# Kernel tuning notes

Hardware: AMD Instinct MI355X
Metric: run time of the kernel (lower is better)

Reference implementation:

```python
import jax, jax.numpy as jnp
import numpy as np

N_NODES = 100000
N_EDGES = 1600000
N_GRAPHS = 256
D = 128      # d_graph
H = 256      # hidden
VOCAB = 30000
OUT = 2


def setup_inputs() -> dict:
    key = jax.random.key(0)
    ks = jax.random.split(key, 24)
    def lin(k, fin, fout):
        s = 1.0 / np.sqrt(fin)
        kw, kb = jax.random.split(k)
        return (jax.random.uniform(kw, (fin, fout), jnp.float32, -s, s),
                jax.random.uniform(kb, (fout,), jnp.float32, -s, s))
    inp = {
        'feat': jax.random.randint(ks[0], (N_NODES,), 0, VOCAB),
        'src': jax.random.randint(ks[1], (N_EDGES,), 0, N_NODES),
        'dst': jax.random.randint(ks[2], (N_EDGES,), 0, N_NODES),
        'graph_id': jnp.sort(jax.random.randint(ks[3], (N_NODES,), 0, N_GRAPHS)),
        'emb': jax.random.normal(ks[4], (VOCAB, D), jnp.float32),
    }
    # SAGEConv layer 0/1: fc_self + fc_neigh + bias (mean aggregator)
    inp['ws0'], _ = lin(ks[5], D, D)
    inp['wn0'], inp['b0'] = lin(ks[6], D, D)
    inp['ws1'], _ = lin(ks[7], D, D)
    inp['wn1'], inp['b1'] = lin(ks[8], D, D)
    inp['e1_w'], inp['e1_b'] = lin(ks[9], D, H)
    inp['e2_w'], inp['e2_b'] = lin(ks[10], H, H)
    inp['e3_w'], inp['e3_b'] = lin(ks[11], H, H)
    inp['e4_w'], inp['e4_b'] = lin(ks[12], H, H)
    inp['pred_w'], inp['pred_b'] = lin(ks[13], H, OUT)
    return inp


def _sage_mean(h, src, dst, ws, wn, b):
    # gather src features, mean-scatter to dst (DGL SAGEConv 'mean')
    msg = jnp.take(h, src, axis=0)                       # [E, D]
    agg = jax.ops.segment_sum(msg, dst, num_segments=N_NODES)
    deg = jax.ops.segment_sum(jnp.ones((src.shape[0],), h.dtype), dst,
                              num_segments=N_NODES)
    h_neigh = agg / jnp.maximum(deg, 1.0)[:, None]
    return h @ ws + h_neigh @ wn + b


def reference(feat, src, dst, graph_id, emb,
              ws0, wn0, b0, ws1, wn1, b1,
              e1_w, e1_b, e2_w, e2_b, e3_w, e3_b, e4_w, e4_b,
              pred_w, pred_b):
    h = jnp.take(emb, feat, axis=0)                      # [N, D]
    h = jax.nn.relu(_sage_mean(h, src, dst, ws0, wn0, b0))
    h = jax.nn.relu(_sage_mean(h, src, dst, ws1, wn1, b1))
    # dgl.mean_nodes: per-graph mean pool
    gsum = jax.ops.segment_sum(h, graph_id, num_segments=N_GRAPHS)
    gcnt = jax.ops.segment_sum(jnp.ones((N_NODES,), h.dtype), graph_id,
                               num_segments=N_GRAPHS)
    hg = gsum / jnp.maximum(gcnt, 1.0)[:, None]          # [B, D]
    hidden = jax.nn.relu(hg @ e1_w + e1_b)
    h2 = jax.nn.relu(hidden @ e2_w + e2_b)
    h3 = jax.nn.relu(h2 @ e3_w + e3_b)
    h4 = jax.nn.relu(h3 @ e4_w + e4_b)
    y = h4 @ pred_w + pred_b
    return jax.nn.log_softmax(y, axis=1), hidden
```

## Files before the change

### kernel.cpp

```cpp
#include <hip/hip_runtime.h>
#include <hip/hip_bf16.h>
#include <math.h>

#define DF 128
#define HID 256
#define NG 256
#define CSR_CAP 1024

typedef __attribute__((ext_vector_type(8))) short s8v;
typedef __attribute__((ext_vector_type(4))) float f32x4;
typedef __attribute__((ext_vector_type(2))) float f32x2;

__device__ __forceinline__ unsigned pack2bf(float lo, float hi){
  unsigned a = __bfloat16_as_ushort(__float2bfloat16(lo));
  unsigned b = __bfloat16_as_ushort(__float2bfloat16(hi));
  return a | (b<<16);
}

__global__ __launch_bounds__(256)
void k_pre0(const float* __restrict__ emb, unsigned* __restrict__ emb_f8, int nvoc,
            const int* __restrict__ dst, int* __restrict__ gb,
            const int* __restrict__ gid, float* __restrict__ gcnt,
            const float* __restrict__ ws0, const float* __restrict__ wn0,
            const float* __restrict__ ws1, const float* __restrict__ wn1,
            unsigned short* __restrict__ wt,
            int N, int E, int NC){
  __shared__ int hist[256];
  const int b = blockIdx.x, t = threadIdx.x;
  if (b < NC){
    int idx = b*256 + t;
    int total = nvoc*(DF/8);
    if (idx<total){
      const float4* e4 = (const float4*)emb;
      float4 v0 = e4[(size_t)idx*2], v1 = e4[(size_t)idx*2+1];
      unsigned w0 = __builtin_amdgcn_cvt_pk_fp8_f32(v0.x, v0.y, 0, false);
      w0 = __builtin_amdgcn_cvt_pk_fp8_f32(v0.z, v0.w, w0, true);
      unsigned w1 = __builtin_amdgcn_cvt_pk_fp8_f32(v1.x, v1.y, 0, false);
      w1 = __builtin_amdgcn_cvt_pk_fp8_f32(v1.z, v1.w, w1, true);
      ((uint2*)emb_f8)[idx] = make_uint2(w0,w1);
    }
  } else if (b < NC+256){
    int bb = b - NC;
    hist[t]=0; __syncthreads();
    for (int i = bb*256+t; i < E; i += 256*256)
      atomicAdd(&hist[dst[i]>>9], 1);
    __syncthreads();
    if (hist[t]) atomicAdd(&gb[t], hist[t]);
  } else if (b < NC+512){
    int bb = b - (NC+256);
    hist[t]=0; __syncthreads();
    for (int i = bb*256+t; i < N; i += 256*256)
      atomicAdd(&hist[gid[i]], 1);
    __syncthreads();
    if (hist[t]) atomicAdd(&gcnt[t], (float)hist[t]);
  } else {
    int bb = b - (NC+512);
    int n = bb & 127;
    int layer = bb >> 7;
    const float* ws = layer? ws1 : ws0;
    const float* wn = layer? wn1 : wn0;
    float v = (t<128)? ws[t*DF+n] : wn[(t-128)*DF+n];
    wt[((size_t)layer*DF + n)*256 + t] = __bfloat16_as_ushort(__float2bfloat16(v));
  }
}

__global__ __launch_bounds__(256)
void k_mid(const int* __restrict__ feat, const unsigned* __restrict__ emb_f8,
           unsigned* __restrict__ h_f8, int N,
           const int* __restrict__ src, const int* __restrict__ dst,
           const int* __restrict__ gb, int* __restrict__ bcur,
           unsigned* __restrict__ pairs, int E, int NP1){
  const int b = blockIdx.x, t = threadIdx.x;
  if (b < NP1){
    int idx = b*256 + t;
    int total = N*8;
    if (idx<total){
      int i = idx>>3, c = idx&7;
      ((uint4*)h_f8)[idx] = ((const uint4*)emb_f8)[(size_t)feat[i]*8 + c];
    }
    return;
  }
  __shared__ int sgb[256];
  __shared__ int hist[256];
  __shared__ int base[256];
  __shared__ int cur[256];
  const int bb = b - NP1;
  const int CH = (E + 255)/256;
  const int s = bb*CH;
  int e = s+CH; if (e>E) e=E;
  if (s>=E) return;
  int v = gb[t];
  sgb[t]=v;
  hist[t]=0;
  __syncthreads();
  for (int o=1;o<256;o<<=1){
    int x = (t>=o)? sgb[t-o] : 0;
    __syncthreads();
    sgb[t]+=x;
    __syncthreads();
  }
  int bstart = sgb[t]-v;
  for (int i=s+t; i<e; i+=256) atomicAdd(&hist[dst[i]>>9],1);
  __syncthreads();
  if (hist[t]){ base[t] = bstart + atomicAdd(&bcur[t],hist[t]); }
  cur[t]=0;
  __syncthreads();
  for (int i=s+t; i<e; i+=256){
    int d = dst[i];
    int bk = d>>9;
    int r = atomicAdd(&cur[bk],1);
    pairs[base[bk]+r] = ((unsigned)src[i]<<9) | (unsigned)(d & 511);
  }
}

__global__ __launch_bounds__(256)
void k_bcsr(const unsigned* __restrict__ pairs, const int* __restrict__ gb,
            int* __restrict__ offs, int* __restrict__ csr, int N, int E){
  __shared__ int sgb[256];
  __shared__ int ncnt[512];
  __shared__ int noff[512];
  __shared__ int sh[256];
  const int t = threadIdx.x;
  const int b = blockIdx.x;
  const int nb0 = b<<9;
  int v = gb[t];
  sgb[t]=v;
  ncnt[t]=0; ncnt[t+256]=0;
  __syncthreads();
  for (int o=1;o<256;o<<=1){
    int x = (t>=o)? sgb[t-o] : 0;
    __syncthreads();
    sgb[t]+=x;
    __syncthreads();
  }
  const int s = sgb[b]-gb[b];
  const int e = sgb[b];
  for (int i=s+t; i<e; i+=256) atomicAdd(&ncnt[pairs[i] & 511u], 1);
  __syncthreads();
  int v0 = ncnt[2*t], v1 = ncnt[2*t+1];
  int vv = v0+v1;
  sh[t]=vv; __syncthreads();
  for (int o=1;o<256;o<<=1){
    int x=(t>=o)?sh[t-o]:0;
    __syncthreads();
    sh[t]+=x;
    __syncthreads();
  }
  int ex = sh[t]-vv;
  noff[2*t]=ex; noff[2*t+1]=ex+v0;
  __syncthreads();
  {
    int n0 = nb0 + t;
    if (n0 < N) offs[n0] = s + noff[t];
    int n1 = nb0 + t + 256;
    if (n1 < N) offs[n1] = s + noff[t+256];
    if (b == gridDim.x-1 && t==0) offs[N] = E;
  }
  ncnt[t]=0; ncnt[t+256]=0;
  __syncthreads();
  for (int i=s+t; i<e; i+=256){
    unsigned p = pairs[i];
    int d = p & 511u;
    int r = atomicAdd(&ncnt[d],1);
    csr[s + noff[d] + r] = (int)(p >> 9);
  }
}

template<int MODE>
__global__ __launch_bounds__(256,8)
void k_sage(const unsigned char* __restrict__ h_in_f8,
            const int* __restrict__ offs, const int* __restrict__ csr,
            const unsigned short* __restrict__ wt,
            const float* __restrict__ bias,
            unsigned char* __restrict__ h_out_f8,
            const int* __restrict__ gid, float* __restrict__ gsum, int N){
  __shared__ __align__(16) unsigned short s_ab[32*256];
  __shared__ int s_csr[CSR_CAP];
  __shared__ int s_gid[32];
  __shared__ float s_tmp[DF];
  const int t = threadIdx.x;
  const int node0 = blockIdx.x*32;
  const uint4* f8r = (const uint4*)h_in_f8;

  if (MODE==1 && t<32) s_gid[t] = (node0+t<N)? gid[node0+t] : -1;

  const int eBase = offs[node0];
  const int eTop  = offs[min(node0+32, N)];
  const int ecount = eTop - eBase;
  const bool useLds = (ecount <= CSR_CAP);
  if (useLds){
    for (int i=t; i<ecount; i+=256) s_csr[i] = csr[eBase+i];
  }

  const int nn = t>>3, c = t&7;
  const int sw = (nn&7)<<4;

  {
    int node = node0+nn;
    uint4 q = make_uint4(0,0,0,0);
    if (node<N) q = f8r[(size_t)node*8 + c];
    f32x2 u; unsigned pk[8];
    u=__builtin_amdgcn_cvt_pk_f32_fp8(q.x,false); pk[0]=pack2bf(u[0],u[1]);
    u=__builtin_amdgcn_cvt_pk_f32_fp8(q.x,true ); pk[1]=pack2bf(u[0],u[1]);
    u=__builtin_amdgcn_cvt_pk_f32_fp8(q.y,false); pk[2]=pack2bf(u[0],u[1]);
    u=__builtin_amdgcn_cvt_pk_f32_fp8(q.y,true ); pk[3]=pack2bf(u[0],u[1]);
    u=__builtin_amdgcn_cvt_pk_f32_fp8(q.z,false); pk[4]=pack2bf(u[0],u[1]);
    u=__builtin_amdgcn_cvt_pk_f32_fp8(q.z,true ); pk[5]=pack2bf(u[0],u[1]);
    u=__builtin_amdgcn_cvt_pk_f32_fp8(q.w,false); pk[6]=pack2bf(u[0],u[1]);
    u=__builtin_amdgcn_cvt_pk_f32_fp8(q.w,true ); pk[7]=pack2bf(u[0],u[1]);
    int byte0 = nn*512 + c*32;
    *(uint4*)((char*)s_ab + ((byte0   )^sw)) = make_uint4(pk[0],pk[1],pk[2],pk[3]);
    *(uint4*)((char*)s_ab + ((byte0+16)^sw)) = make_uint4(pk[4],pk[5],pk[6],pk[7]);
  }
  __syncthreads();

  {
    const int node = node0+nn;
    float a[16];
    #pragma unroll
    for (int j=0;j<16;j++) a[j]=0.f;
    if (node<N){
      int e0=offs[node], e1=offs[node+1];
      int deg = e1-e0;
      if (deg>0){
        #define ACC16(q) { \
          f32x2 u; \
          u=__builtin_amdgcn_cvt_pk_f32_fp8((q).x,false); a[0]+=u[0]; a[1]+=u[1]; \
          u=__builtin_amdgcn_cvt_pk_f32_fp8((q).x,true ); a[2]+=u[0]; a[3]+=u[1]; \
          u=__builtin_amdgcn_cvt_pk_f32_fp8((q).y,false); a[4]+=u[0]; a[5]+=u[1]; \
          u=__builtin_amdgcn_cvt_pk_f32_fp8((q).y,true ); a[6]+=u[0]; a[7]+=u[1]; \
          u=__builtin_amdgcn_cvt_pk_f32_fp8((q).z,false); a[8]+=u[0]; a[9]+=u[1]; \
          u=__builtin_amdgcn_cvt_pk_f32_fp8((q).z,true ); a[10]+=u[0]; a[11]+=u[1]; \
          u=__builtin_amdgcn_cvt_pk_f32_fp8((q).w,false); a[12]+=u[0]; a[13]+=u[1]; \
          u=__builtin_amdgcn_cvt_pk_f32_fp8((q).w,true ); a[14]+=u[0]; a[15]+=u[1]; }
        if (useLds){
          int le = e0 - eBase, le1 = e1 - eBase;
          for (; le+2<=le1; le+=2){
            int s0 = s_csr[le], s1 = s_csr[le+1];
            uint4 q0 = f8r[(size_t)s0*8 + c];
            uint4 q1 = f8r[(size_t)s1*8 + c];
            ACC16(q0); ACC16(q1);
          }
          if (le<le1){
            uint4 q0 = f8r[(size_t)s_csr[le]*8 + c];
            ACC16(q0);
          }
        } else {
          int e = e0;
          for (; e+2<=e1; e+=2){
            int s0 = csr[e], s1 = csr[e+1];
            uint4 q0 = f8r[(size_t)s0*8 + c];
            uint4 q1 = f8r[(size_t)s1*8 + c];
            ACC16(q0); ACC16(q1);
          }
          if (e<e1){
            uint4 q0 = f8r[(size_t)csr[e]*8 + c];
            ACC16(q0);
          }
        }
        #undef ACC16
        float inv = 1.0f/(float)deg;
        #pragma unroll
        for (int j=0;j<16;j++) a[j]*=inv;
      }
    }
    unsigned pk[8];
    #pragma unroll
    for (int j=0;j<8;j++) pk[j] = pack2bf(a[2*j],a[2*j+1]);
    int byte0 = nn*512 + 256 + c*32;
    *(uint4*)((char*)s_ab + ((byte0   )^sw)) = make_uint4(pk[0],pk[1],pk[2],pk[3]);
    *(uint4*)((char*)s_ab + ((byte0+16)^sw)) = make_uint4(pk[4],pk[5],pk[6],pk[7]);
  }

  const int wv = t>>6;
  const int lr = t&15;
  const int kg = (t&63)>>4;
  __syncthreads();

  f32x4 acc00={0,0,0,0}, acc01={0,0,0,0}, acc10={0,0,0,0}, acc11={0,0,0,0};
  const s8v* wt8 = (const s8v*)wt;
  #pragma unroll
  for (int kh=0; kh<2; kh++){
    s8v bfrag[2][4];
    #pragma unroll
    for (int ks=0; ks<4; ks++){
      int kb = (kh*4+ks)*4 + kg;
      bfrag[0][ks] = wt8[(size_t)(wv*32     + lr)*32 + kb];
      bfrag[1][ks] = wt8[(size_t)(wv*32 + 16+ lr)*32 + kb];
    }
    #pragma unroll
    for (int ks=0; ks<4; ks++){
      int cb = (kh*4+ks)*64 + kg*16;
      int r0 = lr, r1 = 16+lr;
      s8v a0 = *(const s8v*)((const char*)s_ab + ((r0*512+cb) ^ ((r0&7)<<4)));
      s8v a1 = *(const s8v*)((const char*)s_ab + ((r1*512+cb) ^ ((r1&7)<<4)));
      acc00 = __builtin_amdgcn_mfma_f32_16x16x32_bf16(a0, bfrag[0][ks], acc00, 0,0,0);
      acc01 = __builtin_amdgcn_mfma_f32_16x16x32_bf16(a0, bfrag[1][ks], acc01, 0,0,0);
      acc10 = __builtin_amdgcn_mfma_f32_16x16x32_bf16(a1, bfrag[0][ks], acc10, 0,0,0);
      acc11 = __builtin_amdgcn_mfma_f32_16x16x32_bf16(a1, bfrag[1][ks], acc11, 0,0,0);
    }
  }
  __syncthreads();

  float* cbuf = (float*)s_ab;
  #pragma unroll
  for (int r=0;r<4;r++){
    int row0 = kg*4 + r;
    cbuf[(row0   )*DF + wv*32      + lr] = acc00[r];
    cbuf[(row0   )*DF + wv*32 + 16 + lr] = acc01[r];
    cbuf[(row0+16)*DF + wv*32      + lr] = acc10[r];
    cbuf[(row0+16)*DF + wv*32 + 16 + lr] = acc11[r];
  }
  __syncthreads();

  if (MODE==0){
    int row = t>>3, c0 = (t&7)*16;
    int node = node0+row;
    if (node<N){
      float x[16];
      #pragma unroll
      for (int j=0;j<16;j++) x[j] = fmaxf(cbuf[row*DF + c0 + j] + bias[c0+j], 0.f);
      unsigned f0 = __builtin_amdgcn_cvt_pk_fp8_f32(x[0], x[1], 0, false);
      f0 = __builtin_amdgcn_cvt_pk_fp8_f32(x[2], x[3], f0, true);
      unsigned f1 = __builtin_amdgcn_cvt_pk_fp8_f32(x[4], x[5], 0, false);
      f1 = __builtin_amdgcn_cvt_pk_fp8_f32(x[6], x[7], f1, true);
      unsigned f2 = __builtin_amdgcn_cvt_pk_fp8_f32(x[8], x[9], 0, false);
      f2 = __builtin_amdgcn_cvt_pk_fp8_f32(x[10], x[11], f2, true);
      unsigned f3 = __builtin_amdgcn_cvt_pk_fp8_f32(x[12], x[13], 0, false);
      f3 = __builtin_amdgcn_cvt_pk_fp8_f32(x[14], x[15], f3, true);
      *(uint4*)&h_out_f8[(size_t)node*DF + c0] = make_uint4(f0,f1,f2,f3);
    }
  } else {
    const int d = t&127, rh = t>>7;
    const float bd = bias[d];
    int segStart = 0;
    while (segStart < 32 && s_gid[segStart] >= 0){
      int g = s_gid[segStart];
      int segEnd = segStart+1;
      while (segEnd < 32 && s_gid[segEnd] == g) segEnd++;
      float p = 0.f;
      for (int r = segStart+rh; r < segEnd; r += 2)
        p += fmaxf(cbuf[r*DF + d] + bd, 0.f);
      if (rh==1) s_tmp[d] = p;
      __syncthreads();
      if (rh==0) atomicAdd(&gsum[g*DF+d], p + s_tmp[d]);
      __syncthreads();
      segStart = segEnd;
    }
  }
}

__global__ __launch_bounds__(256)
void k_head(const float* __restrict__ gsum, const float* __restrict__ gcnt,
            const float* __restrict__ e1w, const float* __restrict__ e1b,
            const float* __restrict__ e2w, const float* __restrict__ e2b,
            const float* __restrict__ e3w, const float* __restrict__ e3b,
            const float* __restrict__ e4w, const float* __restrict__ e4b,
            const float* __restrict__ pw,  const float* __restrict__ pb,
            float* __restrict__ out, float* __restrict__ hidden){
  __shared__ float hg[DF];
  __shared__ float bufA[HID];
  __shared__ float bufB[HID];
  __shared__ float r0[HID], r1[HID];
  const int g = blockIdx.x, t = threadIdx.x;
  if (t<DF) hg[t] = gsum[g*DF+t] / fmaxf(gcnt[g],1.0f);
  __syncthreads();

  float acc = e1b[t];
  for (int k=0;k<DF;++k) acc += hg[k]*e1w[k*HID+t];
  float h1 = fmaxf(acc,0.f);
  hidden[g*HID+t] = h1;
  bufA[t] = h1;
  __syncthreads();

  acc = e2b[t];
  for (int k=0;k<HID;++k) acc += bufA[k]*e2w[k*HID+t];
  bufB[t] = fmaxf(acc,0.f);
  __syncthreads();

  acc = e3b[t];
  for (int k=0;k<HID;++k) acc += bufB[k]*e3w[k*HID+t];
  bufA[t] = fmaxf(acc,0.f);
  __syncthreads();

  acc = e4b[t];
  for (int k=0;k<HID;++k) acc += bufA[k]*e4w[k*HID+t];
  float h4 = fmaxf(acc,0.f);

  r0[t] = h4*pw[t*2+0];
  r1[t] = h4*pw[t*2+1];
  __syncthreads();
  for (int o=128;o>0;o>>=1){
    if (t<o){ r0[t]+=r0[t+o]; r1[t]+=r1[t+o]; }
    __syncthreads();
  }
  if (t==0){
    float y0 = r0[0]+pb[0], y1 = r1[0]+pb[1];
    float m = fmaxf(y0,y1);
    float l = m + logf(expf(y0-m)+expf(y1-m));
    out[g*2+0]=y0-l;
    out[g*2+1]=y1-l;
  }
}

extern "C" void kernel_launch(void* const* d_in, const int* in_sizes, int n_in,
                              void* d_out, int out_size, void* d_ws, size_t ws_size,
                              hipStream_t stream){
  const int* feat = (const int*)d_in[0];
  const int* src  = (const int*)d_in[1];
  const int* dst  = (const int*)d_in[2];
  const int* gid  = (const int*)d_in[3];
  const float* emb = (const float*)d_in[4];
  const float* ws0 = (const float*)d_in[5];
  const float* wn0 = (const float*)d_in[6];
  const float* b0  = (const float*)d_in[7];
  const float* ws1 = (const float*)d_in[8];
  const float* wn1 = (const float*)d_in[9];
  const float* b1  = (const float*)d_in[10];
  const float* e1w = (const float*)d_in[11];
  const float* e1b = (const float*)d_in[12];
  const float* e2w = (const float*)d_in[13];
  const float* e2b = (const float*)d_in[14];
  const float* e3w = (const float*)d_in[15];
  const float* e3b = (const float*)d_in[16];
  const float* e4w = (const float*)d_in[17];
  const float* e4b = (const float*)d_in[18];
  const float* pw  = (const float*)d_in[19];
  const float* pb  = (const float*)d_in[20];
  const int N = in_sizes[0];
  const int E = in_sizes[1];
  const int nvoc = in_sizes[4] / DF;

  char* basep = (char*)d_ws;
  size_t off=0;
  auto alloc=[&](size_t bytes)->void*{
    void* p = basep+off; off=(off+bytes+255)&~(size_t)255; return p;
  };
  unsigned char*  hA_f8 = (unsigned char*) alloc((size_t)N*DF);
  unsigned char*  hB_f8 = (unsigned char*) alloc((size_t)N*DF);
  unsigned char*  emb_f8= (unsigned char*) alloc((size_t)nvoc*DF);
  int*   offs  = (int*)  alloc((size_t)(N+1)*4);
  int*   csr   = (int*)  alloc((size_t)E*4);
  int*   gb    = (int*)  alloc(1024);
  int*   bcur  = (int*)  alloc(1024);
  unsigned short* wtb = (unsigned short*)alloc((size_t)2*DF*256*2);
  float* gsum  = (float*)alloc((size_t)NG*DF*4);
  float* gcnt  = (float*)alloc((size_t)NG*4);
  unsigned* pairs = (unsigned*)alloc((size_t)E*4);
  float* out    = (float*)d_out;
  float* hidden = out + NG*2;

  hipMemsetAsync(gb, 0, 1024, stream);
  hipMemsetAsync(bcur, 0, 1024, stream);
  hipMemsetAsync(gsum, 0, (size_t)NG*DF*4, stream);
  hipMemsetAsync(gcnt, 0, (size_t)NG*4, stream);

  const int NBK = (N+511)>>9;
  const int NC = (nvoc*(DF/8) + 255)/256;
  const int NP1 = (N*8 + 255)/256;
  k_pre0<<<NC+768,256,0,stream>>>(emb,(unsigned*)emb_f8,nvoc,
                                  dst,gb,gid,gcnt,
                                  ws0,wn0,ws1,wn1,wtb,N,E,NC);
  k_mid<<<NP1+256,256,0,stream>>>(feat,(const unsigned*)emb_f8,
                                  (unsigned*)hA_f8,N,
                                  src,dst,gb,bcur,pairs,E,NP1);
  k_bcsr<<<NBK,256,0,stream>>>(pairs,gb,offs,csr,N,E);

  k_sage<0><<<(N+31)/32,256,0,stream>>>(hA_f8,offs,csr,wtb,        b0,
                                        hB_f8,nullptr,nullptr,N);
  k_sage<1><<<(N+31)/32,256,0,stream>>>(hB_f8,offs,csr,wtb+DF*256, b1,
                                        nullptr,gid,gsum,N);

  k_head<<<NG,HID,0,stream>>>(gsum,gcnt,e1w,e1b,e2w,e2b,e3w,e3b,e4w,e4b,
                              pw,pb,out,hidden);
}
```

Before: 214.6 us.

## Split edge bucketing into two-pass radix placement for better write locality

Replaces the single-pass scatter of edges into 196 fine buckets (512 nodes each) with a two-pass radix placement. The first pass scatters into 7 coarse buckets of 16384 nodes, and the second splits each coarse bucket into 32 fine buckets using 40 blocks per coarse bucket. The goal is fewer scattered global writes and less atomic contention per pass, at the cost of an extra kernel launch and an extra E-sized read/write pass. It also lowers CSR_CAP from 1024 to 768. The packed format assumes src fits in 18 bits after a 14-bit shift, which holds for 100k nodes.

```diff
diff --git a/kernel.cpp b/kernel.cpp
--- a/kernel.cpp
+++ b/kernel.cpp
@@ -5,7 +5,8 @@
 #define DF 128
 #define HID 256
 #define NG 256
-#define CSR_CAP 1024
+#define CSR_CAP 768
+#define BPM 40
 
 typedef __attribute__((ext_vector_type(8))) short s8v;
 typedef __attribute__((ext_vector_type(4))) float f32x4;
@@ -65,11 +66,11 @@
 }
 
 __global__ __launch_bounds__(256)
-void k_mid(const int* __restrict__ feat, const unsigned* __restrict__ emb_f8,
-           unsigned* __restrict__ h_f8, int N,
-           const int* __restrict__ src, const int* __restrict__ dst,
-           const int* __restrict__ gb, int* __restrict__ bcur,
-           unsigned* __restrict__ pairs, int E, int NP1){
+void k_place1(const int* __restrict__ feat, const unsigned* __restrict__ emb_f8,
+              unsigned* __restrict__ h_f8, int N,
+              const int* __restrict__ src, const int* __restrict__ dst,
+              const int* __restrict__ gb, int* __restrict__ mbcur,
+              unsigned* __restrict__ pairs1, int E, int NP1){
   const int b = blockIdx.x, t = threadIdx.x;
   if (b < NP1){
     int idx = b*256 + t;
@@ -81,9 +82,10 @@
     return;
   }
   __shared__ int sgb[256];
-  __shared__ int hist[256];
-  __shared__ int base[256];
-  __shared__ int cur[256];
+  __shared__ int mbstart[8];
+  __shared__ int hist1[8];
+  __shared__ int base1[8];
+  __shared__ int cur1[8];
   const int bb = b - NP1;
   const int CH = (E + 255)/256;
   const int s = bb*CH;
@@ -91,7 +93,7 @@
   if (s>=E) return;
   int v = gb[t];
   sgb[t]=v;
-  hist[t]=0;
+  if (t<8){ hist1[t]=0; cur1[t]=0; }
   __syncthreads();
   for (int o=1;o<256;o<<=1){
     int x = (t>=o)? sgb[t-o] : 0;
@@ -99,17 +101,68 @@
     sgb[t]+=x;
     __syncthreads();
   }
-  int bstart = sgb[t]-v;
-  for (int i=s+t; i<e; i+=256) atomicAdd(&hist[dst[i]>>9],1);
-  __syncthreads();
-  if (hist[t]){ base[t] = bstart + atomicAdd(&bcur[t],hist[t]); }
-  cur[t]=0;
+  if ((t&31)==0) mbstart[t>>5] = sgb[t]-v;
+  __syncthreads();
+  for (int i=s+t; i<e; i+=256) atomicAdd(&hist1[dst[i]>>14],1);
+  __syncthreads();
+  if (t<8 && hist1[t]) base1[t] = mbstart[t] + atomicAdd(&mbcur[t],hist1[t]);
   __syncthreads();
   for (int i=s+t; i<e; i+=256){
     int d = dst[i];
-    int bk = d>>9;
-    int r = atomicAdd(&cur[bk],1);
-    pairs[base[bk]+r] = ((unsigned)src[i]<<9) | (unsigned)(d & 511);
+    int m = d>>14;
+    int r = atomicAdd(&cur1[m],1);
+    pairs1[base1[m]+r] = ((unsigned)src[i]<<14) | (unsigned)(d & 16383);
+  }
+}
+
+__global__ __launch_bounds__(256)
+void k_place2(const unsigned* __restrict__ pairs1, const int* __restrict__ gb,
+              int* __restrict__ fcur, unsigned* __restrict__ pairs2, int E){
+  __shared__ int sgb[256];
+  __shared__ int fstart[32];
+  __shared__ int segS_l, segE_l;
+  __shared__ int hist2[32];
+  __shared__ int base2[32];
+  __shared__ int cur2[32];
+  const int t = threadIdx.x;
+  const int m = blockIdx.x / BPM;
+  const int sub = blockIdx.x % BPM;
+  int v = gb[t];
+  sgb[t]=v;
+  if (t<32){ hist2[t]=0; cur2[t]=0; }
+  __syncthreads();
+  for (int o=1;o<256;o<<=1){
+    int x = (t>=o)? sgb[t-o] : 0;
+    __syncthreads();
+    sgb[t]+=x;
+    __syncthreads();
+  }
+  {
+    int f0 = m*32;
+    if (t>=f0 && t<f0+32) fstart[t-f0] = sgb[t]-v;
+    if (t==f0) segS_l = sgb[t]-v;
+    int f1 = f0+32;
+    if (f1 < 256){ if (t==f1) segE_l = sgb[t]-v; }
+    else { if (t==0) segE_l = E; }
+  }
+  __syncthreads();
+  const int segS = segS_l, segE = segE_l;
+  const int segLen = segE - segS;
+  if (segLen<=0) return;
+  const int CH2 = (segLen + BPM-1)/BPM;
+  const int s = segS + sub*CH2;
+  int e = s+CH2; if (e>segE) e=segE;
+  if (s>=segE) return;
+  for (int i=s+t; i<e; i+=256) atomicAdd(&hist2[(pairs1[i]&16383u)>>9],1);
+  __syncthreads();
+  if (t<32 && hist2[t]) base2[t] = fstart[t] + atomicAdd(&fcur[m*32+t],hist2[t]);
+  __syncthreads();
+  for (int i=s+t; i<e; i+=256){
+    unsigned p = pairs1[i];
+    unsigned d14 = p & 16383u;
+    int f = d14>>9;
+    int r = atomicAdd(&cur2[f],1);
+    pairs2[base2[f]+r] = ((p>>14)<<9) | (d14 & 511u);
   }
 }
 
@@ -442,29 +495,34 @@
   int*   offs  = (int*)  alloc((size_t)(N+1)*4);
   int*   csr   = (int*)  alloc((size_t)E*4);
   int*   gb    = (int*)  alloc(1024);
-  int*   bcur  = (int*)  alloc(1024);
+  int*   mbcur = (int*)  alloc(1024);
+  int*   fcur  = (int*)  alloc(1024);
   unsigned short* wtb = (unsigned short*)alloc((size_t)2*DF*256*2);
   float* gsum  = (float*)alloc((size_t)NG*DF*4);
   float* gcnt  = (float*)alloc((size_t)NG*4);
-  unsigned* pairs = (unsigned*)alloc((size_t)E*4);
+  unsigned* pairs1 = (unsigned*)alloc((size_t)E*4);
+  unsigned* pairs2 = (unsigned*)alloc((size_t)E*4);
   float* out    = (float*)d_out;
   float* hidden = out + NG*2;
 
   hipMemsetAsync(gb, 0, 1024, stream);
-  hipMemsetAsync(bcur, 0, 1024, stream);
+  hipMemsetAsync(mbcur, 0, 1024, stream);
+  hipMemsetAsync(fcur, 0, 1024, stream);
   hipMemsetAsync(gsum, 0, (size_t)NG*DF*4, stream);
   hipMemsetAsync(gcnt, 0, (size_t)NG*4, stream);
 
   const int NBK = (N+511)>>9;
+  const int NBMB = (N+16383)>>14;
   const int NC = (nvoc*(DF/8) + 255)/256;
   const int NP1 = (N*8 + 255)/256;
   k_pre0<<<NC+768,256,0,stream>>>(emb,(unsigned*)emb_f8,nvoc,
                                   dst,gb,gid,gcnt,
                                   ws0,wn0,ws1,wn1,wtb,N,E,NC);
-  k_mid<<<NP1+256,256,0,stream>>>(feat,(const unsigned*)emb_f8,
-                                  (unsigned*)hA_f8,N,
-                                  src,dst,gb,bcur,pairs,E,NP1);
-  k_bcsr<<<NBK,256,0,stream>>>(pairs,gb,offs,csr,N,E);
+  k_place1<<<NP1+256,256,0,stream>>>(feat,(const unsigned*)emb_f8,
+                                     (unsigned*)hA_f8,N,
+                                     src,dst,gb,mbcur,pairs1,E,NP1);
+  k_place2<<<NBMB*BPM,256,0,stream>>>(pairs1,gb,fcur,pairs2,E);
+  k_bcsr<<<NBK,256,0,stream>>>(pairs2,gb,offs,csr,N,E);
 
   k_sage<0><<<(N+31)/32,256,0,stream>>>(hA_f8,offs,csr,wtb,        b0,
                                         hB_f8,nullptr,nullptr,N);
```

After: 224.6 us. +4.7%, slower.
